# Performance work log

Measured on AMD Instinct MI355X. Metric: run time of the kernel, lower is better.

## Reference

```python
import jax, jax.numpy as jnp
import numpy as np

B, N, QDIM = 2, 4096, 768
H, D = 8, 64  # num_head, head_dim; inner_dim = 512
INNER = H * D


def setup_inputs() -> dict:
    key = jax.random.key(0)
    ks = jax.random.split(key, 6)
    s = lambda fan_in: 1.0 / np.sqrt(fan_in)
    return {
        "x": jax.random.normal(ks[0], (B, N, QDIM), dtype=jnp.float32),
        "Wq": jax.random.normal(ks[1], (QDIM, INNER), dtype=jnp.float32) * s(QDIM),
        "Wk": jax.random.normal(ks[2], (QDIM, INNER), dtype=jnp.float32) * s(QDIM),
        "Wv": jax.random.normal(ks[3], (QDIM, INNER), dtype=jnp.float32) * s(QDIM),
        "Wout": jax.random.normal(ks[4], (INNER, QDIM), dtype=jnp.float32) * s(INNER),
        "b_out": jnp.zeros((QDIM,), dtype=jnp.float32),
    }


def reference(x, Wq, Wk, Wv, Wout, b_out):
    # x: [b, n, q_dim]; self-attention (kv = x), no mask, dropout = 0 (eval).
    scale = D ** -0.5
    # project and split heads: [b, n, h*d] -> [b, h, n, d]
    def heads(t):
        b, n, _ = t.shape
        return t.reshape(b, n, H, D).transpose(0, 2, 1, 3)
    q = heads(x @ Wq)
    k = heads(x @ Wk)
    v = heads(x @ Wv)
    qk = jnp.einsum("bhid,bhjd->bhij", q, k) * scale  # [b, h, n, n] -- O(n^2) matrix
    attn = jax.nn.softmax(qk, axis=-1)
    out = jnp.einsum("bhij,bhjd->bhid", attn, v)  # [b, h, n, d]
    out = out.transpose(0, 2, 1, 3).reshape(x.shape[0], x.shape[1], INNER)
    return out @ Wout + b_out
```

## Files before the change

### kernel.cpp

```cpp
#include <hip/hip_runtime.h>
#include <cstdint>
#include <cstddef>


typedef __attribute__((ext_vector_type(8))) short short8;
typedef __attribute__((ext_vector_type(4))) float f32x4;
typedef __attribute__((ext_vector_type(16))) float f32x16;
typedef __attribute__((ext_vector_type(4))) unsigned int uint4v;

__device__ __forceinline__ unsigned short f2bf(float f) {
  unsigned int u = __float_as_uint(f);
  u = (u + 0x7fffu + ((u >> 16) & 1u)) >> 16;
  return (unsigned short)u;
}

__device__ __forceinline__ float fast_exp2(float x) {
#if __has_builtin(__builtin_amdgcn_exp2f)
  return __builtin_amdgcn_exp2f(x);
#else
  return __expf(x * 0.69314718055994531f);
#endif
}

__device__ __forceinline__ void gld16(const void* g, void* l) {
  __builtin_amdgcn_global_load_lds(
      (__attribute__((address_space(1))) void*)const_cast<void*>(g),
      (__attribute__((address_space(3))) void*)l, 16, 0, 0);
}

__device__ __forceinline__ unsigned int cvtpk_bf16(float lo, float hi) {
  unsigned int r;
  asm("v_cvt_pk_bf16_f32 %0, %1, %2" : "=v"(r) : "v"(lo), "v"(hi));
  return r;
}


__global__ __launch_bounds__(256) void cvt_x_k(const float* __restrict__ x,
                                               unsigned short* __restrict__ xb) {
  const size_t i = ((size_t)blockIdx.x * 256 + threadIdx.x) * 4;
  const float4 v = *(const float4*)(x + i);
  ushort4 u;
  u.x = f2bf(v.x); u.y = f2bf(v.y); u.z = f2bf(v.z); u.w = f2bf(v.w);
  *(ushort4*)(xb + i) = u;
}

__global__ __launch_bounds__(256) void transpose_w_k(
    const float* __restrict__ Wq, const float* __restrict__ Wk,
    const float* __restrict__ Wv, const float* __restrict__ Wout,
    unsigned short* __restrict__ Wt,
    unsigned short* __restrict__ WoT)
{
  __shared__ float t[32][33];
  const int z = blockIdx.z;
  const float* src = (z == 0) ? Wq : (z == 1) ? Wk : (z == 2) ? Wv : Wout;
  const int R = (z < 3) ? 768 : 512, C = (z < 3) ? 512 : 768;
  unsigned short* dst = (z < 3) ? (Wt + (size_t)z * 393216) : WoT;
  const int tx = threadIdx.x & 31, ty = threadIdx.x >> 5;
  const int c0 = blockIdx.x * 32, r0 = blockIdx.y * 32;
  if (c0 >= C || r0 >= R) return;
#pragma unroll
  for (int k = 0; k < 4; ++k)
    t[ty + 8 * k][tx] = src[(size_t)(r0 + ty + 8 * k) * C + c0 + tx];
  __syncthreads();
#pragma unroll
  for (int k = 0; k < 4; ++k)
    dst[(size_t)(c0 + ty + 8 * k) * R + r0 + tx] = f2bf(t[tx][ty + 8 * k]);
}


__global__ __launch_bounds__(256) void gemm_qkv_k(
    const unsigned short* __restrict__ A,
    const unsigned short* __restrict__ Wt,
    unsigned short* __restrict__ qb, unsigned short* __restrict__ kb,
    unsigned short* __restrict__ vtb) {
  __shared__ __align__(16) short Al[4096];
  __shared__ __align__(16) short Bl[4096];
  const int tid = threadIdx.x;
  const int w = tid >> 6, lane = tid & 63, quad = lane >> 4, l15 = lane & 15;
  const int wy = w >> 1, wx = w & 1;
  const int m0 = blockIdx.x * 128, n0 = blockIdx.y * 128;
  const int z = blockIdx.z;
  const unsigned short* Bt = Wt + (size_t)z * (512 * 768);

  f32x4 acc[4][4];
#pragma unroll
  for (int i = 0; i < 4; ++i)
#pragma unroll
    for (int j = 0; j < 4; ++j) acc[i][j] = (f32x4){0.f, 0.f, 0.f, 0.f};

  for (int k0 = 0; k0 < 768; k0 += 32) {
    __syncthreads();
#pragma unroll
    for (int s = 0; s < 2; ++s) {
      const int t = s * 256 + tid;
      gld16(A + (size_t)(m0 + (t >> 2)) * 768 + k0 + (t & 3) * 8,
            Al + s * 2048 + w * 512);
      gld16(Bt + (size_t)(n0 + (t >> 2)) * 768 + k0 + (t & 3) * 8,
            Bl + s * 2048 + w * 512);
    }
    __syncthreads();
    short8 af[4], bf[4];
#pragma unroll
    for (int i = 0; i < 4; ++i) {
      af[i] = *(const short8*)(Al + (wy * 64 + i * 16 + l15) * 32 + quad * 8);
      bf[i] = *(const short8*)(Bl + (wx * 64 + i * 16 + l15) * 32 + quad * 8);
    }
    if (z == 2) {
#pragma unroll
      for (int i = 0; i < 4; ++i)
#pragma unroll
        for (int j = 0; j < 4; ++j)
          acc[i][j] = __builtin_amdgcn_mfma_f32_16x16x32_bf16(af[i], bf[j], acc[i][j], 0, 0, 0);
    } else {
#pragma unroll
      for (int i = 0; i < 4; ++i)
#pragma unroll
        for (int j = 0; j < 4; ++j)
          acc[i][j] = __builtin_amdgcn_mfma_f32_16x16x32_bf16(bf[i], af[j], acc[i][j], 0, 0, 0);
    }
  }

  if (z == 2) {
#pragma unroll
    for (int i = 0; i < 4; ++i) {
#pragma unroll
      for (int j = 0; j < 4; ++j) {
        const int m0r = m0 + wy * 64 + i * 16 + quad * 4;
        const int n = n0 + wx * 64 + j * 16 + l15;
        const int b = m0r >> 12, nseq0 = m0r & 4095;
        const int h = n >> 6, d0 = n & 63;
        const int kti = nseq0 >> 5, kc = (nseq0 >> 4) & 1;
        const int hv = (nseq0 >> 2) & 1;
        const int e0 = ((nseq0 >> 3) & 1) * 4;
        const int dt = (d0 >> 5) & 1, lv = hv * 32 + (d0 & 31);
        ushort4 u;
        u.x = f2bf(acc[i][j][0]); u.y = f2bf(acc[i][j][1]);
        u.z = f2bf(acc[i][j][2]); u.w = f2bf(acc[i][j][3]);
        *(ushort4*)(vtb + (size_t)(b * 8 + h) * 262144 +
                    ((((kti * 2 + dt) * 2 + kc) * 64 + lv) * 8 + e0)) = u;
      }
    }
  } else {
    const float qs = 0.18033688011112042f;
#pragma unroll
    for (int i = 0; i < 4; ++i) {
#pragma unroll
      for (int j = 0; j < 4; ++j) {
        const int n0r = n0 + wx * 64 + i * 16 + quad * 4;
        const int m = m0 + wy * 64 + j * 16 + l15;
        const int b = m >> 12, nseq = m & 4095;
        const int h = n0r >> 6, d0 = n0r & 63;
        ushort4 u;
        if (z == 0) {
          u.x = f2bf(acc[i][j][0] * qs); u.y = f2bf(acc[i][j][1] * qs);
          u.z = f2bf(acc[i][j][2] * qs); u.w = f2bf(acc[i][j][3] * qs);
          *(ushort4*)(qb + (size_t)((b * 8 + h) * 4096 + nseq) * 64 + d0) = u;
        } else {
          const int kti = nseq >> 5, l31k = nseq & 31;
          const int c = (d0 >> 4) & 3, hk = (d0 >> 3) & 1, e0 = d0 & 7;
          u.x = f2bf(acc[i][j][0]); u.y = f2bf(acc[i][j][1]);
          u.z = f2bf(acc[i][j][2]); u.w = f2bf(acc[i][j][3]);
          *(ushort4*)(kb + (size_t)(b * 8 + h) * 262144 +
                      (((kti * 4 + c) * 64 + (hk * 32 + l31k)) * 8 + e0)) = u;
        }
      }
    }
  }
}


__global__ __launch_bounds__(256) void attn_k(
    const unsigned short* __restrict__ qb,
    const unsigned short* __restrict__ kb,
    const unsigned short* __restrict__ vtb,
    unsigned short* __restrict__ ob) {
  __shared__ __align__(16) char smem[34816];
  const int tid = threadIdx.x;
  const int w = tid >> 6, lane = tid & 63;
  const int l31 = lane & 31, hi = lane >> 5;
  const int g = w >> 1, wq = w & 1;

  const int L = blockIdx.x + 32 * blockIdx.y;
  const int bh = ((L & 7) << 1) | ((L >> 3) & 1);
  const int q0 = (L >> 4) << 7;

  const unsigned short* qbase = qb + (size_t)bh * (4096 * 64);
  const unsigned short* kbase = kb + (size_t)bh * 262144 + lane * 8;
  const unsigned short* vbase = vtb + (size_t)bh * 262144 + lane * 8;

  short8 qf[2][4];
#pragma unroll
  for (int qs = 0; qs < 2; ++qs) {
    const int qrow = q0 + wq * 64 + qs * 32 + l31;
#pragma unroll
    for (int c = 0; c < 4; ++c)
      qf[qs][c] = *(const short8*)(qbase + (size_t)qrow * 64 + c * 16 + hi * 8);
  }

  f32x16 Oacc[2][2];
#pragma unroll
  for (int qs = 0; qs < 2; ++qs)
#pragma unroll
    for (int dt = 0; dt < 2; ++dt)
#pragma unroll
      for (int r = 0; r < 16; ++r) Oacc[qs][dt][r] = 0.f;
  float lsum[2] = {0.f, 0.f};

  const int jbase = g * 2048;

  for (int j0 = 0; j0 < 2048; j0 += 64) {
    const int kti0 = (jbase + j0) >> 5;
#pragma unroll
    for (int kt = 0; kt < 2; ++kt) {
      const int kti = kti0 + kt;
      short8 kf[4];
#pragma unroll
      for (int c = 0; c < 4; ++c)
        kf[c] = *(const short8*)(kbase + (size_t)(kti * 4 + c) * 512);
      short8 vf[2][2];
#pragma unroll
      for (int dt = 0; dt < 2; ++dt)
#pragma unroll
        for (int kc = 0; kc < 2; ++kc)
          vf[dt][kc] = *(const short8*)(vbase + (size_t)((kti * 2 + dt) * 2 + kc) * 512);

      uint4v pa[2][2];
#pragma unroll
      for (int qs = 0; qs < 2; ++qs) {
        f32x16 s;
#pragma unroll
        for (int r = 0; r < 16; ++r) s[r] = 0.f;
        __builtin_amdgcn_s_setprio(1);
#pragma unroll
        for (int c = 0; c < 4; ++c)
          s = __builtin_amdgcn_mfma_f32_32x32x16_bf16(kf[c], qf[qs][c], s, 0, 0, 0);
        __builtin_amdgcn_s_setprio(0);

        float e[16];
#pragma unroll
        for (int r = 0; r < 16; ++r) e[r] = fast_exp2(s[r]);
        lsum[qs] += (((e[0] + e[1]) + (e[2] + e[3])) + ((e[4] + e[5]) + (e[6] + e[7]))) +
                    (((e[8] + e[9]) + (e[10] + e[11])) + ((e[12] + e[13]) + (e[14] + e[15])));

        unsigned int wv[8];
#pragma unroll
        for (int g2 = 0; g2 < 4; ++g2)
#pragma unroll
          for (int p = 0; p < 2; ++p)
            wv[g2 * 2 + p] = cvtpk_bf16(e[4 * g2 + 2 * p], e[4 * g2 + 2 * p + 1]);

        pa[qs][0] = (uint4v){wv[0], wv[1], wv[2], wv[3]};
        pa[qs][1] = (uint4v){wv[4], wv[5], wv[6], wv[7]};
      }

      __builtin_amdgcn_s_setprio(1);
#pragma unroll
      for (int dt = 0; dt < 2; ++dt)
#pragma unroll
        for (int kc = 0; kc < 2; ++kc)
#pragma unroll
          for (int qs = 0; qs < 2; ++qs)
            Oacc[qs][dt] = __builtin_amdgcn_mfma_f32_32x32x16_bf16(
                __builtin_bit_cast(short8, pa[qs][kc]), vf[dt][kc], Oacc[qs][dt], 0, 0, 0);
      __builtin_amdgcn_s_setprio(0);
    }
  }

  float lt[2];
#pragma unroll
  for (int qs = 0; qs < 2; ++qs)
    lt[qs] = lsum[qs] + __shfl_xor(lsum[qs], 32, 64);

  __syncthreads();
  float* Ox = (float*)smem;
  float* Lx = (float*)(smem + 33792);
#pragma unroll
  for (int qs = 0; qs < 2; ++qs)
    Lx[g * 128 + wq * 64 + qs * 32 + l31] = lt[qs];
  if (g == 1) {
#pragma unroll
    for (int qs = 0; qs < 2; ++qs)
#pragma unroll
      for (int dt = 0; dt < 2; ++dt)
#pragma unroll
        for (int r = 0; r < 16; ++r) {
          const int row = wq * 64 + qs * 32 + (r & 3) + 8 * (r >> 2) + 4 * hi;
          Ox[row * 66 + dt * 32 + l31] = Oacc[qs][dt][r];
        }
  }
  __syncthreads();
  if (g == 0) {
    const int b = bh >> 3, h = bh & 7;
#pragma unroll
    for (int qs = 0; qs < 2; ++qs)
#pragma unroll
      for (int r = 0; r < 16; ++r) {
        const int row = wq * 64 + qs * 32 + (r & 3) + 8 * (r >> 2) + 4 * hi;
        const float inv = 1.0f / (Lx[row] + Lx[128 + row]);
#pragma unroll
        for (int dt = 0; dt < 2; ++dt)
          ob[(size_t)(b * 4096 + q0 + row) * 512 + h * 64 + dt * 32 + l31] =
              f2bf((Oacc[qs][dt][r] + Ox[row * 66 + dt * 32 + l31]) * inv);
      }
  }
}


__global__ __launch_bounds__(256) void gemm_out_k(
    const unsigned short* __restrict__ A,
    const unsigned short* __restrict__ Bt,
    const float* __restrict__ bias, float* __restrict__ out) {
  __shared__ __align__(16) short Al[4096];
  __shared__ __align__(16) short Bl[2048];
  const int tid = threadIdx.x;
  const int w = tid >> 6, lane = tid & 63, quad = lane >> 4, l15 = lane & 15;
  const int m0 = blockIdx.x * 128, n0 = blockIdx.y * 64;

  f32x4 acc[2][4];
#pragma unroll
  for (int i = 0; i < 2; ++i)
#pragma unroll
    for (int j = 0; j < 4; ++j) acc[i][j] = (f32x4){0.f, 0.f, 0.f, 0.f};

  for (int k0 = 0; k0 < 512; k0 += 32) {
    __syncthreads();
#pragma unroll
    for (int s = 0; s < 2; ++s) {
      const int t = s * 256 + tid;
      gld16(A + (size_t)(m0 + (t >> 2)) * 512 + k0 + (t & 3) * 8,
            Al + s * 2048 + w * 512);
    }
    gld16(Bt + (size_t)(n0 + (tid >> 2)) * 512 + k0 + (tid & 3) * 8,
          Bl + w * 512);
    __syncthreads();
    short8 af[2], bf[4];
#pragma unroll
    for (int i = 0; i < 2; ++i)
      af[i] = *(const short8*)(Al + (w * 32 + i * 16 + l15) * 32 + quad * 8);
#pragma unroll
    for (int j = 0; j < 4; ++j)
      bf[j] = *(const short8*)(Bl + (j * 16 + l15) * 32 + quad * 8);
#pragma unroll
    for (int i = 0; i < 2; ++i)
#pragma unroll
      for (int j = 0; j < 4; ++j)
        acc[i][j] = __builtin_amdgcn_mfma_f32_16x16x32_bf16(bf[j], af[i], acc[i][j], 0, 0, 0);
  }

#pragma unroll
  for (int i = 0; i < 2; ++i) {
#pragma unroll
    for (int j = 0; j < 4; ++j) {
      const int col0 = n0 + j * 16 + quad * 4;
      const int m = m0 + w * 32 + i * 16 + l15;
      const float4 b4 = *(const float4*)(bias + col0);
      float4 o;
      o.x = acc[i][j][0] + b4.x; o.y = acc[i][j][1] + b4.y;
      o.z = acc[i][j][2] + b4.z; o.w = acc[i][j][3] + b4.w;
      *(float4*)(out + (size_t)m * 768 + col0) = o;
    }
  }
}


extern "C" void kernel_launch(void* const* d_in, const int* in_sizes, int n_in,
                              void* d_out, int out_size, void* d_ws, size_t ws_size,
                              hipStream_t stream) {
  const float* x    = (const float*)d_in[0];
  const float* Wq   = (const float*)d_in[1];
  const float* Wk   = (const float*)d_in[2];
  const float* Wv   = (const float*)d_in[3];
  const float* Wout = (const float*)d_in[4];
  const float* bout = (const float*)d_in[5];
  float* out = (float*)d_out;
  char* ws = (char*)d_ws;

  unsigned short* xb  = (unsigned short*)(ws);
  unsigned short* Wt  = (unsigned short*)(ws + 12582912);
  unsigned short* WoT = (unsigned short*)(ws + 14942208);
  unsigned short* qb  = (unsigned short*)(ws + 15728640);
  unsigned short* kb  = (unsigned short*)(ws + 24117248);
  unsigned short* vtb = (unsigned short*)(ws + 32505856);
  unsigned short* ob  = (unsigned short*)(ws + 40894464);

  cvt_x_k<<<6144, 256, 0, stream>>>(x, xb);
  transpose_w_k<<<dim3(24, 24, 4), 256, 0, stream>>>(Wq, Wk, Wv, Wout, Wt, WoT);
  gemm_qkv_k<<<dim3(64, 4, 3), 256, 0, stream>>>(xb, Wt, qb, kb, vtb);
  attn_k<<<dim3(32, 16), 256, 0, stream>>>(qb, kb, vtb, ob);
  gemm_out_k<<<dim3(64, 12), 256, 0, stream>>>(ob, WoT, bout, out);
}
```

Before: 217.2 us.

## Split attention over key halves with separate merge kernel

Adds a split-K attention kernel that launches twice as many blocks, each covering half of the key sequence and writing fp32 partial outputs and row sums to workspace. A separate merge kernel adds the two halves, normalizes them and converts to bf16. The aim is more blocks to fill the GPU's compute units better. In exchange it adds a large fp32 round trip through global memory and an extra kernel launch. It runs only when the workspace is large enough.

```diff
diff --git a/kernel.cpp b/kernel.cpp
--- a/kernel.cpp
+++ b/kernel.cpp
@@ -306,6 +306,166 @@
 }
 
 
+__global__ __launch_bounds__(256, 4) void attn_split_k(
+    const unsigned short* __restrict__ qb,
+    const unsigned short* __restrict__ kb,
+    const unsigned short* __restrict__ vtb,
+    float* __restrict__ Op,
+    float* __restrict__ Lp) {
+  __shared__ __align__(16) char smem[34816];
+  const int tid = threadIdx.x;
+  const int w = tid >> 6, lane = tid & 63;
+  const int l31 = lane & 31, hi = lane >> 5;
+  const int g = w >> 1, wq = w & 1;
+
+  const int L = blockIdx.x + 64 * blockIdx.y;
+  const int bh = ((L & 7) << 1) | ((L >> 3) & 1);
+  const int q0 = ((L >> 4) & 31) << 7;
+  const int kgB = (L >> 9) & 1;
+
+  const unsigned short* qbase = qb + (size_t)bh * (4096 * 64);
+  const unsigned short* kbase = kb + (size_t)bh * 262144 + lane * 8;
+  const unsigned short* vbase = vtb + (size_t)bh * 262144 + lane * 8;
+
+  short8 qf[2][4];
+#pragma unroll
+  for (int qs = 0; qs < 2; ++qs) {
+    const int qrow = q0 + wq * 64 + qs * 32 + l31;
+#pragma unroll
+    for (int c = 0; c < 4; ++c)
+      qf[qs][c] = *(const short8*)(qbase + (size_t)qrow * 64 + c * 16 + hi * 8);
+  }
+
+  f32x16 Oacc[2][2];
+#pragma unroll
+  for (int qs = 0; qs < 2; ++qs)
+#pragma unroll
+    for (int dt = 0; dt < 2; ++dt)
+#pragma unroll
+      for (int r = 0; r < 16; ++r) Oacc[qs][dt][r] = 0.f;
+  float lsum[2] = {0.f, 0.f};
+
+  const int jbase = kgB * 2048 + g * 1024;
+
+  for (int j0 = 0; j0 < 1024; j0 += 64) {
+    const int kti0 = (jbase + j0) >> 5;
+#pragma unroll
+    for (int kt = 0; kt < 2; ++kt) {
+      const int kti = kti0 + kt;
+      short8 kf[4];
+#pragma unroll
+      for (int c = 0; c < 4; ++c)
+        kf[c] = *(const short8*)(kbase + (size_t)(kti * 4 + c) * 512);
+      short8 vf[2][2];
+#pragma unroll
+      for (int dt = 0; dt < 2; ++dt)
+#pragma unroll
+        for (int kc = 0; kc < 2; ++kc)
+          vf[dt][kc] = *(const short8*)(vbase + (size_t)((kti * 2 + dt) * 2 + kc) * 512);
+
+      uint4v pa[2][2];
+#pragma unroll
+      for (int qs = 0; qs < 2; ++qs) {
+        f32x16 s;
+#pragma unroll
+        for (int r = 0; r < 16; ++r) s[r] = 0.f;
+        __builtin_amdgcn_s_setprio(1);
+#pragma unroll
+        for (int c = 0; c < 4; ++c)
+          s = __builtin_amdgcn_mfma_f32_32x32x16_bf16(kf[c], qf[qs][c], s, 0, 0, 0);
+        __builtin_amdgcn_s_setprio(0);
+
+        float e[16];
+#pragma unroll
+        for (int r = 0; r < 16; ++r) e[r] = fast_exp2(s[r]);
+        lsum[qs] += (((e[0] + e[1]) + (e[2] + e[3])) + ((e[4] + e[5]) + (e[6] + e[7]))) +
+                    (((e[8] + e[9]) + (e[10] + e[11])) + ((e[12] + e[13]) + (e[14] + e[15])));
+
+        unsigned int wv[8];
+#pragma unroll
+        for (int g2 = 0; g2 < 4; ++g2)
+#pragma unroll
+          for (int p = 0; p < 2; ++p)
+            wv[g2 * 2 + p] = cvtpk_bf16(e[4 * g2 + 2 * p], e[4 * g2 + 2 * p + 1]);
+
+        pa[qs][0] = (uint4v){wv[0], wv[1], wv[2], wv[3]};
+        pa[qs][1] = (uint4v){wv[4], wv[5], wv[6], wv[7]};
+      }
+
+      __builtin_amdgcn_s_setprio(1);
+#pragma unroll
+      for (int dt = 0; dt < 2; ++dt)
+#pragma unroll
+        for (int kc = 0; kc < 2; ++kc)
+#pragma unroll
+          for (int qs = 0; qs < 2; ++qs)
+            Oacc[qs][dt] = __builtin_amdgcn_mfma_f32_32x32x16_bf16(
+                __builtin_bit_cast(short8, pa[qs][kc]), vf[dt][kc], Oacc[qs][dt], 0, 0, 0);
+      __builtin_amdgcn_s_setprio(0);
+    }
+  }
+
+  float lt[2];
+#pragma unroll
+  for (int qs = 0; qs < 2; ++qs)
+    lt[qs] = lsum[qs] + __shfl_xor(lsum[qs], 32, 64);
+
+  __syncthreads();
+  float* Ox = (float*)smem;
+  float* Lx = (float*)(smem + 33792);
+#pragma unroll
+  for (int qs = 0; qs < 2; ++qs)
+    Lx[g * 128 + wq * 64 + qs * 32 + l31] = lt[qs];
+  if (g == 1) {
+#pragma unroll
+    for (int qs = 0; qs < 2; ++qs)
+#pragma unroll
+      for (int dt = 0; dt < 2; ++dt)
+#pragma unroll
+        for (int r = 0; r < 16; ++r) {
+          const int row = wq * 64 + qs * 32 + (r & 3) + 8 * (r >> 2) + 4 * hi;
+          Ox[row * 66 + dt * 32 + l31] = Oacc[qs][dt][r];
+        }
+  }
+  __syncthreads();
+  if (g == 0) {
+    const int b = bh >> 3, h = bh & 7;
+    float* OpH = Op + (size_t)kgB * 4194304;
+    float* LpH = Lp + (size_t)kgB * 65536;
+#pragma unroll
+    for (int qs = 0; qs < 2; ++qs)
+#pragma unroll
+      for (int r = 0; r < 16; ++r) {
+        const int row = wq * 64 + qs * 32 + (r & 3) + 8 * (r >> 2) + 4 * hi;
+        LpH[bh * 4096 + q0 + row] = Lx[row] + Lx[128 + row];
+#pragma unroll
+        for (int dt = 0; dt < 2; ++dt)
+          OpH[(size_t)(b * 4096 + q0 + row) * 512 + h * 64 + dt * 32 + l31] =
+              Oacc[qs][dt][r] + Ox[row * 66 + dt * 32 + l31];
+      }
+  }
+}
+
+__global__ __launch_bounds__(256) void merge_attn_k(
+    const float* __restrict__ Op, const float* __restrict__ Lp,
+    unsigned short* __restrict__ ob) {
+  const size_t t = (size_t)blockIdx.x * 256 + threadIdx.x;
+  const size_t i4 = t * 4;
+  const int qrow = (int)(i4 >> 9);
+  const int col = (int)(i4 & 511);
+  const int h = col >> 6;
+  const int b = qrow >> 12, q = qrow & 4095;
+  const float4 a = *(const float4*)(Op + i4);
+  const float4 c = *(const float4*)(Op + 4194304 + i4);
+  const int li = (b * 8 + h) * 4096 + q;
+  const float inv = 1.0f / (Lp[li] + Lp[65536 + li]);
+  ushort4 u;
+  u.x = f2bf((a.x + c.x) * inv); u.y = f2bf((a.y + c.y) * inv);
+  u.z = f2bf((a.z + c.z) * inv); u.w = f2bf((a.w + c.w) * inv);
+  *(ushort4*)(ob + i4) = u;
+}
+
+
 __global__ __launch_bounds__(256) void gemm_out_k(
     const unsigned short* __restrict__ A,
     const unsigned short* __restrict__ Bt,
@@ -382,10 +542,17 @@
   unsigned short* kb  = (unsigned short*)(ws + 24117248);
   unsigned short* vtb = (unsigned short*)(ws + 32505856);
   unsigned short* ob  = (unsigned short*)(ws + 40894464);
+  float* Op = (float*)(ws + 49283072);
+  float* Lp = (float*)(ws + 82837504);
 
   cvt_x_k<<<6144, 256, 0, stream>>>(x, xb);
   transpose_w_k<<<dim3(24, 24, 4), 256, 0, stream>>>(Wq, Wk, Wv, Wout, Wt, WoT);
   gemm_qkv_k<<<dim3(64, 4, 3), 256, 0, stream>>>(xb, Wt, qb, kb, vtb);
-  attn_k<<<dim3(32, 16), 256, 0, stream>>>(qb, kb, vtb, ob);
+  if (ws_size >= 83361792u) {
+    attn_split_k<<<dim3(64, 16), 256, 0, stream>>>(qb, kb, vtb, Op, Lp);
+    merge_attn_k<<<4096, 256, 0, stream>>>(Op, Lp, ob);
+  } else {
+    attn_k<<<dim3(32, 16), 256, 0, stream>>>(qb, kb, vtb, ob);
+  }
   gemm_out_k<<<dim3(64, 12), 256, 0, stream>>>(ob, WoT, bout, out);
 }
```

Result: slower. 820.7 us (+277.9%).
